# Optimization experiments

Hardware: AMD Instinct MI355X
Metric: run time of the kernel (lower is better)

Reference implementation:

```python
import jax, jax.numpy as jnp
import numpy as np
from jax import lax

B, T, L, OUT, SP, E, H = 128, 300, 28, 28, 7, 20, 256
W = T - L + 1          # 273 sliding windows
W_OUT = W - OUT        # 245 training windows
F_IN = L + 1 + E       # 49 rnn input features


def _lstm_dilated(x, d, Wih, Whh, b):
    # x: [T0, B, F]; dilation d realized by phase-stacking time into batch (zalando DRNN scheme)
    T0, Bn, F = x.shape
    pad = (-T0) % d
    if pad:
        x = jnp.concatenate([x, jnp.zeros((pad, Bn, F), x.dtype)], axis=0)
    Tn = x.shape[0] // d
    xd = x.reshape(Tn, d * Bn, F)  # element [k, j*Bn:(j+1)*Bn] == x[k*d+j]
    Hh = Whh.shape[1]

    def step(carry, xt):
        h, c = carry
        z = xt @ Wih.T + h @ Whh.T + b
        i, f, g, o = jnp.split(z, 4, axis=-1)  # torch LSTM gate order i,f,g,o
        c = jax.nn.sigmoid(f) * c + jax.nn.sigmoid(i) * jnp.tanh(g)
        h = jax.nn.sigmoid(o) * jnp.tanh(c)
        return (h, c), h

    h0 = jnp.zeros((d * Bn, Hh), x.dtype)
    _, hs = lax.scan(step, (h0, h0), xd)
    return hs.reshape(Tn * d, Bn, Hh)[:T0]


def _forward(train_dataset, val_dataset, alpha_raw, gamma_raw, init_seas,
             input_categories, my_param,
             Wih1, Whh1, b1, Wih2, Whh2, b2, Wih3, Whh3, b3, Wih4, Whh4, b4,
             linear_W, linear_b, score_W, score_b):
    x = train_dataset
    a = jax.nn.sigmoid(alpha_raw)   # [B]
    g = jax.nn.sigmoid(gamma_raw)   # [B]
    S0 = jnp.exp(init_seas)         # [B,7] = seasonalities[0..6]
    s7 = S0[:, 0]                   # seasonalities[7] = exp(init[:,0])
    level0 = x[:, 0] / S0[:, 0]
    buf0 = jnp.concatenate([S0[:, 1:], s7[:, None]], axis=1)  # S[1..7], shift register

    def es_step(carry, xt):
        level, buf = carry
        s = buf[:, 0]
        lvl = a * (xt / s) + (1.0 - a) * level
        s_new = g * (xt / lvl) + (1.0 - g) * s
        buf = jnp.concatenate([buf[:, 1:], s_new[:, None]], axis=1)
        return (lvl, buf), (lvl, s_new)

    _, (lvls, s_news) = lax.scan(es_step, (level0, buf0), x[:, 1:].T)
    levels = jnp.concatenate([level0[None], lvls], axis=0).T        # [B,T]
    S_full = jnp.concatenate([S0, s7[:, None], s_news.T], axis=1)   # [B,T+7]
    # extension: cat(S_full, S_full[:, T : T-7+28])  -> [B, T+28]
    S_ext = jnp.concatenate([S_full, S_full[:, T:T - SP + OUT]], axis=1)

    # input windows (vectorized over all W window positions)
    widx = jnp.arange(W)[:, None] + jnp.arange(L)[None, :]          # [W,L]
    lvl_w = levels[:, L - 1 + jnp.arange(W)]                        # [B,W]
    norm_in = x[:, widx] / S_ext[:, widx] / lvl_w[:, :, None]       # [B,W,L]
    cats = jnp.broadcast_to(input_categories[:, None, :], (B, W, E))
    cat_in = jnp.concatenate([norm_in, cats], axis=2)[jnp.arange(B) % 10]  # original j%10 row pick
    mp = jnp.broadcast_to(my_param.reshape(1, 1, 1), (B, W, 1))
    window_input = jnp.transpose(jnp.concatenate([cat_in, mp], axis=2), (1, 0, 2))  # [W,B,F_IN]

    # output windows
    oidx = (L + jnp.arange(W_OUT))[:, None] + jnp.arange(OUT)[None, :]  # [W_OUT,OUT]
    lvl_o = levels[:, L - 1 + jnp.arange(W_OUT)]                        # [B,W_OUT]
    window_output = jnp.transpose(x[:, oidx] / S_ext[:, oidx] / lvl_o[:, :, None], (1, 0, 2))

    # residual dilated LSTM stack: block1 dilations (1,2); block2 dilations (2,6) + residual
    h1 = _lstm_dilated(window_input, 1, Wih1, Whh1, b1)
    h1 = _lstm_dilated(h1, 2, Wih2, Whh2, b2)
    h2 = _lstm_dilated(h1, 2, Wih3, Whh3, b3)
    h2 = _lstm_dilated(h2, 6, Wih4, Whh4, b4) + h1
    h = jnp.tanh(h2 @ linear_W.T + linear_b)
    rnn_out = h @ score_W.T + score_b                                   # [W,B,OUT]

    # LSTM stack is causal, so running on window_input[:-OUT] equals slicing the full run
    prediction_values = rnn_out[:-OUT]
    actual_values = window_output
    holdout = rnn_out[-1] * S_ext[:, -OUT:] * levels[:, -1:]
    holdout_prediction = holdout * (holdout > 0).astype(holdout.dtype)
    hav = val_dataset
    hav_norm = hav / S_ext[:, -OUT:] / levels[:, -1:]
    return (prediction_values, actual_values, holdout_prediction, rnn_out, hav, hav_norm)


def setup_inputs() -> dict:
    key = jax.random.key(0)
    ks = jax.random.split(key, 24)
    s = float(1.0 / np.sqrt(H))
    u = lambda k, shape: jax.random.uniform(k, shape, jnp.float32, -s, s)
    inp = {
        "train_dataset": jax.random.uniform(ks[0], (B, T), jnp.float32) * 2.0 + 0.5,  # positive sales
        "val_dataset": jax.random.uniform(ks[1], (B, OUT), jnp.float32) * 2.0 + 0.5,
        "alpha_raw": jnp.full((B,), 0.5, jnp.float32),
        "gamma_raw": jnp.full((B,), 0.5, jnp.float32),
        "init_seas": jnp.full((B, SP), 0.5, jnp.float32),
        "input_categories": jnp.full((B, E), 0.001, jnp.float32) + 0.01 * jax.random.normal(ks[2], (B, E), jnp.float32),
        "my_param": jnp.full((1,), 0.001, jnp.float32),
        "Wih1": u(ks[3], (4 * H, F_IN)), "Whh1": u(ks[4], (4 * H, H)), "b1": u(ks[5], (4 * H,)),
        "Wih2": u(ks[6], (4 * H, H)), "Whh2": u(ks[7], (4 * H, H)), "b2": u(ks[8], (4 * H,)),
        "Wih3": u(ks[9], (4 * H, H)), "Whh3": u(ks[10], (4 * H, H)), "b3": u(ks[11], (4 * H,)),
        "Wih4": u(ks[12], (4 * H, H)), "Whh4": u(ks[13], (4 * H, H)), "b4": u(ks[14], (4 * H,)),
        "linear_W": u(ks[15], (H, H)), "linear_b": u(ks[16], (H,)),
        "score_W": u(ks[17], (OUT, H)), "score_b": u(ks[18], (OUT,)),
    }
    return inp


def reference(train_dataset, val_dataset, alpha_raw, gamma_raw, init_seas,
              input_categories, my_param,
              Wih1, Whh1, b1, Wih2, Whh2, b2, Wih3, Whh3, b3, Wih4, Whh4, b4,
              linear_W, linear_b, score_W, score_b):
    return _forward(train_dataset, val_dataset, alpha_raw, gamma_raw, init_seas,
                    input_categories, my_param,
                    Wih1, Whh1, b1, Wih2, Whh2, b2, Wih3, Whh3, b3, Wih4, Whh4, b4,
                    linear_W, linear_b, score_W, score_b)
```

## Files before the change

kernel.cpp:

```cpp
#include <hip/hip_runtime.h>

typedef unsigned int u32;

static __device__ __forceinline__ float sigf (float x){ return 1.0f/(1.0f+__expf(-x)); }
static __device__ __forceinline__ float tanh_(float x){ return 2.0f/(1.0f+__expf(-2.0f*x)) - 1.0f; }

#define NM 2730
#define N_O0 878080

static __device__ __forceinline__ int dot4(u32 a, u32 b, int acc){
#if __has_builtin(__builtin_amdgcn_sdot4)
  return __builtin_amdgcn_sdot4((int)a, (int)b, acc, false);
#else
  int s = acc;
  #pragma unroll
  for(int i=0;i<4;i++){
    int av = (int)((signed char)((a >> (8*i)) & 0xffu));
    int bv = (int)((signed char)((b >> (8*i)) & 0xffu));
    s += av*bv;
  }
  return s;
#endif
}

__global__ __launch_bounds__(256) void k_prep(
    const float* __restrict__ x,     float* __restrict__ xT,
    const float* __restrict__ wi0,   float* __restrict__ wT0,
    const float* __restrict__ wi1,   float* __restrict__ wT1,
    const float* __restrict__ wi2,   float* __restrict__ wT2,
    const float* __restrict__ wi3,   float* __restrict__ wT3,
    const float* __restrict__ lw,    float* __restrict__ lwT,
    const float* __restrict__ sw,    float* __restrict__ swT,
    const float* __restrict__ h0, const float* __restrict__ h1,
    const float* __restrict__ h2, const float* __restrict__ h3,
    float* __restrict__ zsc){
  int i = blockIdx.x*256 + threadIdx.x;
  if(i < 38400){
    int t = i >> 7, b = i & 127;
    xT[i] = x[b*300 + t];
    return;
  }
  i -= 38400;
  if(i < 50176){ int c=i/1024, r=i-c*1024; wT0[i] = wi0[r*49 + c];  return; }
  i -= 50176;
  if(i < 262144){ int c=i>>10, r=i&1023; wT1[i] = wi1[r*256 + c];   return; }
  i -= 262144;
  if(i < 262144){ int c=i>>10, r=i&1023; wT2[i] = wi2[r*256 + c];   return; }
  i -= 262144;
  if(i < 262144){ int c=i>>10, r=i&1023; wT3[i] = wi3[r*256 + c];   return; }
  i -= 262144;
  if(i < 65536){ int c=i>>8, r=i&255; lwT[i] = lw[r*256 + c];       return; }
  i -= 65536;
  if(i < 7168){ int c=i/28, r=i-c*28; swT[i] = sw[r*256 + c];       return; }
  i -= 7168;
  if(i < 4096){
    int l = i >> 10, r = i & 1023;
    const float* W = (l==0)?h0:(l==1)?h1:(l==2)?h2:h3;
    const float4* p = (const float4*)(W + (size_t)r*256);
    float m = 0.f;
    #pragma unroll 8
    for(int q=0;q<64;q++){
      float4 v = p[q];
      m = fmaxf(m, fmaxf(fmaxf(fabsf(v.x),fabsf(v.y)), fmaxf(fabsf(v.z),fabsf(v.w))));
    }
    zsc[i] = fmaxf(m, 1e-20f) * (1.0f/16129.0f);
  }
}

__global__ __launch_bounds__(256) void k_packes(
    const float* __restrict__ h0, const float* __restrict__ h1,
    const float* __restrict__ h2, const float* __restrict__ h3,
    const float* __restrict__ zsc, u32* __restrict__ W8,
    const float* __restrict__ xT, const float* __restrict__ alpha,
    const float* __restrict__ gamma, const float* __restrict__ iseas,
    float* __restrict__ ST, float* __restrict__ lvlT){
  __shared__ float xs[128*301];
  if(blockIdx.x < 1024){
    int i = blockIdx.x*256 + threadIdx.x;
    int l = i >> 16;
    int uidx = i & 65535;
    int dw = uidx & 3;
    int kg = (uidx >> 2) & 127;
    int q  = (uidx >> 9) & 3;
    int rr = (uidx >> 11) & 7;
    int js = uidx >> 14;
    int row = rr*128 + kg;
    int k0  = js*64 + q*16 + dw*4;
    const float* W = (l==0)?h0:(l==1)?h1:(l==2)?h2:h3;
    float inv = 1.0f / (zsc[l*1024 + row] * 127.0f);
    u32 out = 0;
    #pragma unroll
    for(int b=0;b<4;b++){
      float v = W[(size_t)row*256 + k0 + b];
      int q8 = max(-127, min(127, __float2int_rn(v * inv)));
      out |= ((u32)(q8 & 0xff)) << (8*b);
    }
    W8[i] = out;
    return;
  }
  for(int i=threadIdx.x; i<38400; i+=256){
    int t = i >> 7, b = i & 127;
    xs[b*301 + t] = xT[i];
  }
  __syncthreads();
  int b = threadIdx.x;
  if(b >= 128) return;
  float a = sigf(alpha[b]);
  float g = sigf(gamma[b]);
  float S0[7];
  #pragma unroll
  for(int i=0;i<7;i++){ S0[i] = __expf(iseas[b*7+i]); ST[i*128+b] = S0[i]; }
  ST[7*128+b] = S0[0];
  float q0=S0[1],q1=S0[2],q2=S0[3],q3=S0[4],q4=S0[5],q5=S0[6],q6=S0[0];
  float lvl = xs[b*301]/S0[0];
  lvlT[b] = lvl;
  for(int t=1;t<300;t++){
    float xt = xs[b*301 + t];
    float s  = q0;
    lvl = a*(xt/s) + (1.0f-a)*lvl;
    float sn = g*(xt/lvl) + (1.0f-g)*s;
    q0=q1;q1=q2;q2=q3;q3=q4;q4=q5;q5=q6;q6=sn;
    lvlT[t*128+b]   = lvl;
    ST[(t+7)*128+b] = sn;
  }
}

__global__ __launch_bounds__(256) void k_gemm1(
    const float* __restrict__ xT, const float* __restrict__ ST,
    const float* __restrict__ lvlT, const float* __restrict__ cats,
    const float* __restrict__ mp,
    const float* __restrict__ WT,
    const float* __restrict__ bias,
    float* __restrict__ Z){
  __shared__ float Xs[8][52];
  const int tid = threadIdx.x;
  const int m0 = blockIdx.x*8;
  for(int idx=tid; idx<8*49; idx+=256){
    int p = idx/49, f = idx - p*49;
    int m = m0+p;
    float v = 0.f;
    if(m < NM){
      int tt = m/10, jj = m - (m/10)*10;
      if(f < 28){
        int c = tt + f;
        v = xT[c*128 + jj] / ST[c*128 + jj] / lvlT[(tt+27)*128 + jj];
      } else if(f < 48){
        v = cats[jj*20 + (f-28)];
      } else {
        v = mp[0];
      }
    }
    Xs[p][f] = v;
  }
  __syncthreads();
  float acc0[8], acc1[8], acc2[8], acc3[8];
  {
    float b0 = bias[tid];
    float b1 = bias[tid+256];
    float b2 = bias[tid+512];
    float b3 = bias[tid+768];
    #pragma unroll
    for(int p=0;p<8;p++){ acc0[p]=b0; acc1[p]=b1; acc2[p]=b2; acc3[p]=b3; }
  }
  #pragma unroll 7
  for(int f=0; f<49; f++){
    float w0 = WT[f*1024 + tid      ];
    float w1 = WT[f*1024 + tid+256  ];
    float w2 = WT[f*1024 + tid+512  ];
    float w3 = WT[f*1024 + tid+768  ];
    #pragma unroll
    for(int p=0;p<8;p++){
      float xv = Xs[p][f];
      acc0[p] += w0*xv; acc1[p] += w1*xv; acc2[p] += w2*xv; acc3[p] += w3*xv;
    }
  }
  for(int p=0;p<8;p++){
    int m = m0+p;
    if(m < NM){
      float* zb = Z + m*1024 + tid;
      zb[0]=acc0[p]; zb[256]=acc1[p]; zb[512]=acc2[p]; zb[768]=acc3[p];
    }
  }
}

__global__ __launch_bounds__(256) void k_gemm(const float* __restrict__ X,
                                              const float* __restrict__ WT,
                                              const float* __restrict__ bias,
                                              float* __restrict__ Z){
  __shared__ float Xs[8][256];
  const int tid = threadIdx.x;
  const int m0 = blockIdx.x*8;
  for(int p=0;p<8;p++){
    int m = m0+p;
    Xs[p][tid] = (m < NM) ? X[m*256+tid] : 0.0f;
  }
  __syncthreads();
  float acc0[8], acc1[8], acc2[8], acc3[8];
  {
    float b0 = bias[tid];
    float b1 = bias[tid+256];
    float b2 = bias[tid+512];
    float b3 = bias[tid+768];
    #pragma unroll
    for(int p=0;p<8;p++){ acc0[p]=b0; acc1[p]=b1; acc2[p]=b2; acc3[p]=b3; }
  }
  #pragma unroll 4
  for(int f=0; f<256; f++){
    float w0 = WT[f*1024 + tid      ];
    float w1 = WT[f*1024 + tid+256  ];
    float w2 = WT[f*1024 + tid+512  ];
    float w3 = WT[f*1024 + tid+768  ];
    #pragma unroll
    for(int p=0;p<8;p++){
      float xv = Xs[p][f];
      acc0[p] += w0*xv; acc1[p] += w1*xv; acc2[p] += w2*xv; acc3[p] += w3*xv;
    }
  }
  for(int p=0;p<8;p++){
    int m = m0+p;
    if(m < NM){
      float* zb = Z + m*1024 + tid;
      zb[0]=acc0[p]; zb[256]=acc1[p]; zb[512]=acc2[p]; zb[768]=acc3[p];
    }
  }
}

__global__ __launch_bounds__(512) void k_scan8(
    const float* __restrict__ Z,
    const u32* __restrict__ W8,
    const float* __restrict__ zsc,
    float* __restrict__ Y,
    const float* __restrict__ RES,
    int d){
  __shared__ __align__(16) u32 h8[64];
  __shared__ int   zp[4][1024];
  __shared__ float sc[1024];
  const int tid = threadIdx.x;
  const int chain = blockIdx.x;
  const int j = chain % 10;
  const int r = chain / 10;
  const int ns = (273 - r + d - 1)/d;
  const int kg = tid & 127;
  const int js = tid >> 7;
  const uint4* Wb = (const uint4*)W8 + (size_t)js*4096 + kg;
  const uint4* hq = (const uint4*)h8 + js*4;

  for(int i=tid;i<1024;i+=512) sc[i] = zsc[i];
  if(tid < 64) h8[tid] = 0u;
  float cst = 0.0f;
  __syncthreads();

  int t = r;
  for(int s=0; s<ns; s++, t+=d){
    const size_t row = (size_t)(t*10 + j);
    float zv0=0.f, zv1=0.f, zv2=0.f, zv3=0.f, rv=0.f;
    if(tid < 256){
      const float* zb = Z + row*1024;
      zv0 = zb[tid]; zv1 = zb[tid+256]; zv2 = zb[tid+512]; zv3 = zb[tid+768];
      if(RES) rv = RES[row*256 + tid];
    }
    int a0=0,a1=0,a2=0,a3=0,a4=0,a5=0,a6=0,a7=0;
    #pragma unroll
    for(int q=0;q<4;q++){
      uint4 h4 = hq[q];
      #pragma unroll
      for(int rr=0;rr<8;rr++){
        uint4 w = Wb[rr*512 + q*128];
        int* ap = (rr==0)?&a0:(rr==1)?&a1:(rr==2)?&a2:(rr==3)?&a3:
                  (rr==4)?&a4:(rr==5)?&a5:(rr==6)?&a6:&a7;
        int acc = *ap;
        acc = dot4(w.x, h4.x, acc);
        acc = dot4(w.y, h4.y, acc);
        acc = dot4(w.z, h4.z, acc);
        acc = dot4(w.w, h4.w, acc);
        *ap = acc;
      }
    }
    zp[js][       kg] = a0;
    zp[js][128  + kg] = a1;
    zp[js][256  + kg] = a2;
    zp[js][384  + kg] = a3;
    zp[js][512  + kg] = a4;
    zp[js][640  + kg] = a5;
    zp[js][768  + kg] = a6;
    zp[js][896  + kg] = a7;
    __syncthreads();
    if(tid < 256){
      const int u = tid;
      int si = zp[0][u]     + zp[1][u]     + zp[2][u]     + zp[3][u];
      int sf = zp[0][u+256] + zp[1][u+256] + zp[2][u+256] + zp[3][u+256];
      int sg = zp[0][u+512] + zp[1][u+512] + zp[2][u+512] + zp[3][u+512];
      int so = zp[0][u+768] + zp[1][u+768] + zp[2][u+768] + zp[3][u+768];
      float zi = zv0 + sc[u]     * (float)si;
      float zf = zv1 + sc[u+256] * (float)sf;
      float zg = zv2 + sc[u+512] * (float)sg;
      float zo = zv3 + sc[u+768] * (float)so;
      float c  = sigf(zf)*cst + sigf(zi)*tanh_(zg);
      float h  = sigf(zo)*tanh_(c);
      cst = c;
      int hqi = __float2int_rn(h * 127.0f);
      hqi = max(-127, min(127, hqi));
      ((signed char*)h8)[u] = (signed char)hqi;
      Y[row*256 + u] = h + rv;
    }
    asm volatile("s_waitcnt lgkmcnt(0)\n\ts_barrier" ::: "memory");
  }
}

__global__ __launch_bounds__(256) void k_head(const float* __restrict__ Y4,
    const float* __restrict__ LWT,
    const float* __restrict__ lb,
    const float* __restrict__ SWT,
    const float* __restrict__ sb,
    float* __restrict__ rnnS){
  __shared__ float v [8][256];
  __shared__ float h2[8][256];
  const int tid = threadIdx.x;
  const int m0 = blockIdx.x*8;
  for(int p=0;p<8;p++){
    int m = m0+p;
    v[p][tid] = (m<NM) ? Y4[m*256+tid] : 0.0f;
  }
  __syncthreads();
  float acc[8];
  float bz = lb[tid];
  #pragma unroll
  for(int p=0;p<8;p++) acc[p]=bz;
  #pragma unroll 4
  for(int f=0; f<256; f++){
    float w = LWT[f*256+tid];
    #pragma unroll
    for(int p=0;p<8;p++) acc[p] += w * v[p][f];
  }
  #pragma unroll
  for(int p=0;p<8;p++) h2[p][tid] = tanh_(acc[p]);
  __syncthreads();
  if(tid < 224){
    int o = tid % 28, p = tid / 28;
    int m = m0 + p;
    if(m < NM){
      float a = sb[o];
      for(int f=0; f<256; f++) a += SWT[f*28+o] * h2[p][f];
      rnnS[m*28 + o] = a;
    }
  }
}

__global__ __launch_bounds__(256) void k_outs(
    const float* __restrict__ rnnS, const float* __restrict__ ST,
    const float* __restrict__ lvlT, const float* __restrict__ xT,
    const float* __restrict__ val,  float* __restrict__ out,
    int nblk){
  const int tid = threadIdx.x;
  const int bid = blockIdx.x;
  if(bid < 245){
    __shared__ float av[28*132];
    const int t = bid;
    for(int i=tid; i<28*128; i+=256){
      int o = i >> 7, b = i & 127;
      int c = 28 + t + o;
      av[o*132 + b] = xT[c*128+b] / ST[c*128+b] / lvlT[(27+t)*128+b];
    }
    __syncthreads();
    for(int i=tid; i<3584; i+=256){
      int b = i/28, o = i - b*28;
      out[878080 + t*3584 + i] = av[o*132 + b];
    }
    return;
  }
  const int stride = (nblk - 245)*256;
  for(int i0 = (bid-245)*256 + tid; i0 < 978432 + 3584 + 3584; i0 += stride){
    int i = i0;
    if(i < 978432){
      int t = i/3584; int rr = i - t*3584;
      int b = rr/28;  int o = rr - b*28;
      int j = b % 10;
      float a = rnnS[(t*10 + j)*28 + o];
      out[1759744 + i] = a;
      if(t < 245) out[i] = a;
    } else { i -= 978432;
      if(i < 3584){
        int b = i/28, o = i - (i/28)*28;
        int j = b % 10;
        float a = rnnS[(2720 + j)*28 + o];
        int col = (o < 21) ? (286+o) : (279+o);
        float hv = a * ST[col*128 + b] * lvlT[299*128 + b];
        out[1756160 + i] = (hv > 0.0f) ? hv : 0.0f;
      } else { i -= 3584;
        int b = i/28, o = i - (i/28)*28;
        int col = (o < 21) ? (286+o) : (279+o);
        float Sm = ST[col*128 + b];
        float lv = lvlT[299*128 + b];
        out[2738176 + i] = val[i];
        out[2741760 + i] = val[i] / Sm / lv;
      }
    }
  }
}

extern "C" void kernel_launch(void* const* d_in, const int* in_sizes, int n_in,
                              void* d_out, int out_size, void* d_ws, size_t ws_size,
                              hipStream_t stream){
  (void)in_sizes; (void)n_in; (void)out_size; (void)ws_size;
  const float* x     = (const float*)d_in[0];
  const float* val   = (const float*)d_in[1];
  const float* alpha = (const float*)d_in[2];
  const float* gamma = (const float*)d_in[3];
  const float* iseas = (const float*)d_in[4];
  const float* cats  = (const float*)d_in[5];
  const float* mp    = (const float*)d_in[6];
  const float* Wih[4]  = {(const float*)d_in[7],  (const float*)d_in[10], (const float*)d_in[13], (const float*)d_in[16]};
  const float* Whh[4]  = {(const float*)d_in[8],  (const float*)d_in[11], (const float*)d_in[14], (const float*)d_in[17]};
  const float* bias[4] = {(const float*)d_in[9],  (const float*)d_in[12], (const float*)d_in[15], (const float*)d_in[18]};
  const float* linW  = (const float*)d_in[19];
  const float* linb  = (const float*)d_in[20];
  const float* scW   = (const float*)d_in[21];
  const float* scb   = (const float*)d_in[22];

  float* Fw   = (float*)d_ws;
  float* ST   = Fw;
  float* lvlT = ST   + 39296;
  float* xT   = lvlT + 38400;
  float* xz   = xT   + 38400;
  float* yA   = xz   + 2795520;
  float* yB   = yA   + 698880;
  float* wihT[4];
  wihT[0] = yB + 698880;
  wihT[1] = wihT[0] + 50176;
  wihT[2] = wihT[1] + 262144;
  wihT[3] = wihT[2] + 262144;
  float* linWT = wihT[3] + 262144;
  float* scT   = linWT + 65536;
  float* zsc   = scT   + 7168;
  u32*   W8all = (u32*)(zsc + 4096);
  float* rnnS  = (float*)(W8all + 262144);

  k_prep<<<3718, 256, 0, stream>>>(x, xT,
      Wih[0], wihT[0], Wih[1], wihT[1], Wih[2], wihT[2], Wih[3], wihT[3],
      linW, linWT, scW, scT,
      Whh[0], Whh[1], Whh[2], Whh[3], zsc);

  k_packes<<<1025, 256, 0, stream>>>(Whh[0], Whh[1], Whh[2], Whh[3], zsc, W8all,
                                     xT, alpha, gamma, iseas, ST, lvlT);

  const int    dlt[4]    = {1, 2, 2, 6};
  const int    chains[4] = {10, 20, 20, 60};
  const float* Xin[4]    = {nullptr, yA, yB, yA};
  float*       Yout[4]   = {yA, yB, yA, yA};
  for(int l=0;l<4;l++){
    if(l == 0)
      k_gemm1<<<(NM+7)/8, 256, 0, stream>>>(xT, ST, lvlT, cats, mp,
                                            wihT[0], bias[0], xz);
    else
      k_gemm<<<(NM+7)/8, 256, 0, stream>>>(Xin[l], wihT[l], bias[l], xz);
    k_scan8<<<chains[l], 512, 0, stream>>>(xz, W8all + l*65536, zsc + l*1024,
                                           Yout[l],
                                           (l==3) ? yB : (const float*)nullptr, dlt[l]);
  }

  k_head<<<(NM+7)/8, 256, 0, stream>>>(yA, linWT, linb, scT, scb, rnnS);
  const int nblk = 245 + 1024;
  k_outs<<<nblk, 256, 0, stream>>>(rnnS, ST, lvlT, xT, val, (float*)d_out, nblk);
}
```

Measured before the change: 958.6 us.

## Fuse prep kernels, merge per-layer GEMM and scan with flag sync

Measured after the change: 1.026 ms. +7.0%, slower.

```diff
diff --git a/kernel.cpp b/kernel.cpp
--- a/kernel.cpp
+++ b/kernel.cpp
@@ -23,220 +23,195 @@
 #endif
 }
 
-__global__ __launch_bounds__(256) void k_prep(
-    const float* __restrict__ x,     float* __restrict__ xT,
-    const float* __restrict__ wi0,   float* __restrict__ wT0,
-    const float* __restrict__ wi1,   float* __restrict__ wT1,
-    const float* __restrict__ wi2,   float* __restrict__ wT2,
-    const float* __restrict__ wi3,   float* __restrict__ wT3,
-    const float* __restrict__ lw,    float* __restrict__ lwT,
-    const float* __restrict__ sw,    float* __restrict__ swT,
+__global__ __launch_bounds__(256) void k_prepall(
+    const float* __restrict__ x,
+    const float* __restrict__ alpha, const float* __restrict__ gamma,
+    const float* __restrict__ iseas,
+    const float* __restrict__ wi0, const float* __restrict__ wi1,
+    const float* __restrict__ wi2, const float* __restrict__ wi3,
+    const float* __restrict__ lw,  const float* __restrict__ sw,
     const float* __restrict__ h0, const float* __restrict__ h1,
     const float* __restrict__ h2, const float* __restrict__ h3,
-    float* __restrict__ zsc){
-  int i = blockIdx.x*256 + threadIdx.x;
-  if(i < 38400){
-    int t = i >> 7, b = i & 127;
-    xT[i] = x[b*300 + t];
+    float* __restrict__ xT,  float* __restrict__ wT0, float* __restrict__ wT1,
+    float* __restrict__ wT2, float* __restrict__ wT3,
+    float* __restrict__ lwT, float* __restrict__ swT,
+    float* __restrict__ zsc, u32* __restrict__ W8,
+    float* __restrict__ ST, float* __restrict__ lvlT,
+    u32* __restrict__ flags){
+  __shared__ float xs[128*61];
+  const int tid = threadIdx.x;
+  const int bid = blockIdx.x;
+  if(bid == 0){
+    int b = tid;
+    float a=0.f, g=0.f, lvl=0.f;
+    float q0=0,q1=0,q2=0,q3=0,q4=0,q5=0,q6=0;
+    if(tid < 128){
+      a = sigf(alpha[b]);
+      g = sigf(gamma[b]);
+      float S0[7];
+      #pragma unroll
+      for(int i=0;i<7;i++){ S0[i] = __expf(iseas[b*7+i]); ST[i*128+b] = S0[i]; }
+      ST[7*128+b] = S0[0];
+      q0=S0[1];q1=S0[2];q2=S0[3];q3=S0[4];q4=S0[5];q5=S0[6];q6=S0[0];
+      lvl = 0.f;
+      (void)lvl;
+    }
+    for(int c=0;c<5;c++){
+      __syncthreads();
+      for(int i=tid; i<128*60; i+=256){
+        int bb = i/60, tt = i - bb*60;
+        xs[bb*61 + tt] = x[bb*300 + c*60 + tt];
+      }
+      __syncthreads();
+      if(tid < 128){
+        int tt0 = 0;
+        if(c == 0){
+          lvl = xs[b*61] / q6;
+          lvlT[b] = lvl;
+          tt0 = 1;
+        }
+        for(int tt=tt0; tt<60; tt++){
+          int t = c*60 + tt;
+          float xt = xs[b*61 + tt];
+          float s  = q0;
+          lvl = a*(xt/s) + (1.0f-a)*lvl;
+          float sn = g*(xt/lvl) + (1.0f-g)*s;
+          q0=q1;q1=q2;q2=q3;q3=q4;q4=q5;q5=q6;q6=sn;
+          lvlT[t*128+b]   = lvl;
+          ST[(t+7)*128+b] = sn;
+        }
+      }
+    }
     return;
   }
+  if(bid <= 1024){
+    if(bid == 1 && tid < 4) flags[tid] = 0u;
+    int gid  = (bid-1)*4 + (tid >> 6);
+    int lane = tid & 63;
+    int l    = gid >> 10;
+    int row  = gid & 1023;
+    const float* W = (l==0)?h0:(l==1)?h1:(l==2)?h2:h3;
+    float4 v = ((const float4*)(W + (size_t)row*256))[lane];
+    float m = fmaxf(fmaxf(fabsf(v.x),fabsf(v.y)), fmaxf(fabsf(v.z),fabsf(v.w)));
+    #pragma unroll
+    for(int d=1; d<64; d<<=1) m = fmaxf(m, __shfl_xor(m, d));
+    float zv = fmaxf(m, 1e-20f) * (1.0f/16129.0f);
+    if(lane == 0) zsc[gid] = zv;
+    float inv = 1.0f / (zv * 127.0f);
+    u32 out = 0;
+    {
+      float vv[4] = {v.x, v.y, v.z, v.w};
+      #pragma unroll
+      for(int bq=0;bq<4;bq++){
+        int q8 = max(-127, min(127, __float2int_rn(vv[bq] * inv)));
+        out |= ((u32)(q8 & 0xff)) << (8*bq);
+      }
+    }
+    int js = lane >> 4, q = (lane >> 2) & 3, dw = lane & 3;
+    W8[(size_t)l*65536 + js*16384 + (row>>7)*2048 + q*512 + (row&127)*4 + dw] = out;
+    return;
+  }
+  int i = (bid-1025)*256 + tid;
+  if(i < 38400){ int t=i>>7, b=i&127; xT[i] = x[b*300+t]; return; }
   i -= 38400;
-  if(i < 50176){ int c=i/1024, r=i-c*1024; wT0[i] = wi0[r*49 + c];  return; }
+  if(i < 50176){ int c=i/1024, r=i-c*1024; wT0[i] = wi0[r*49+c]; return; }
   i -= 50176;
-  if(i < 262144){ int c=i>>10, r=i&1023; wT1[i] = wi1[r*256 + c];   return; }
+  if(i < 262144){ int c=i>>10, r=i&1023; wT1[i] = wi1[r*256+c]; return; }
   i -= 262144;
-  if(i < 262144){ int c=i>>10, r=i&1023; wT2[i] = wi2[r*256 + c];   return; }
+  if(i < 262144){ int c=i>>10, r=i&1023; wT2[i] = wi2[r*256+c]; return; }
   i -= 262144;
-  if(i < 262144){ int c=i>>10, r=i&1023; wT3[i] = wi3[r*256 + c];   return; }
+  if(i < 262144){ int c=i>>10, r=i&1023; wT3[i] = wi3[r*256+c]; return; }
   i -= 262144;
-  if(i < 65536){ int c=i>>8, r=i&255; lwT[i] = lw[r*256 + c];       return; }
+  if(i < 65536){ int c=i>>8, r=i&255; lwT[i] = lw[r*256+c]; return; }
   i -= 65536;
-  if(i < 7168){ int c=i/28, r=i-c*28; swT[i] = sw[r*256 + c];       return; }
-  i -= 7168;
-  if(i < 4096){
-    int l = i >> 10, r = i & 1023;
-    const float* W = (l==0)?h0:(l==1)?h1:(l==2)?h2:h3;
-    const float4* p = (const float4*)(W + (size_t)r*256);
-    float m = 0.f;
-    #pragma unroll 8
-    for(int q=0;q<64;q++){
-      float4 v = p[q];
-      m = fmaxf(m, fmaxf(fmaxf(fabsf(v.x),fabsf(v.y)), fmaxf(fabsf(v.z),fabsf(v.w))));
-    }
-    zsc[i] = fmaxf(m, 1e-20f) * (1.0f/16129.0f);
-  }
-}
-
-__global__ __launch_bounds__(256) void k_packes(
-    const float* __restrict__ h0, const float* __restrict__ h1,
-    const float* __restrict__ h2, const float* __restrict__ h3,
-    const float* __restrict__ zsc, u32* __restrict__ W8,
-    const float* __restrict__ xT, const float* __restrict__ alpha,
-    const float* __restrict__ gamma, const float* __restrict__ iseas,
-    float* __restrict__ ST, float* __restrict__ lvlT){
-  __shared__ float xs[128*301];
-  if(blockIdx.x < 1024){
-    int i = blockIdx.x*256 + threadIdx.x;
-    int l = i >> 16;
-    int uidx = i & 65535;
-    int dw = uidx & 3;
-    int kg = (uidx >> 2) & 127;
-    int q  = (uidx >> 9) & 3;
-    int rr = (uidx >> 11) & 7;
-    int js = uidx >> 14;
-    int row = rr*128 + kg;
-    int k0  = js*64 + q*16 + dw*4;
-    const float* W = (l==0)?h0:(l==1)?h1:(l==2)?h2:h3;
-    float inv = 1.0f / (zsc[l*1024 + row] * 127.0f);
-    u32 out = 0;
-    #pragma unroll
-    for(int b=0;b<4;b++){
-      float v = W[(size_t)row*256 + k0 + b];
-      int q8 = max(-127, min(127, __float2int_rn(v * inv)));
-      out |= ((u32)(q8 & 0xff)) << (8*b);
-    }
-    W8[i] = out;
-    return;
-  }
-  for(int i=threadIdx.x; i<38400; i+=256){
-    int t = i >> 7, b = i & 127;
-    xs[b*301 + t] = xT[i];
-  }
-  __syncthreads();
-  int b = threadIdx.x;
-  if(b >= 128) return;
-  float a = sigf(alpha[b]);
-  float g = sigf(gamma[b]);
-  float S0[7];
-  #pragma unroll
-  for(int i=0;i<7;i++){ S0[i] = __expf(iseas[b*7+i]); ST[i*128+b] = S0[i]; }
-  ST[7*128+b] = S0[0];
-  float q0=S0[1],q1=S0[2],q2=S0[3],q3=S0[4],q4=S0[5],q5=S0[6],q6=S0[0];
-  float lvl = xs[b*301]/S0[0];
-  lvlT[b] = lvl;
-  for(int t=1;t<300;t++){
-    float xt = xs[b*301 + t];
-    float s  = q0;
-    lvl = a*(xt/s) + (1.0f-a)*lvl;
-    float sn = g*(xt/lvl) + (1.0f-g)*s;
-    q0=q1;q1=q2;q2=q3;q3=q4;q4=q5;q5=q6;q6=sn;
-    lvlT[t*128+b]   = lvl;
-    ST[(t+7)*128+b] = sn;
-  }
-}
-
-__global__ __launch_bounds__(256) void k_gemm1(
+  if(i < 7168){ int c=i/28, r=i-c*28; swT[i] = sw[r*256+c]; }
+}
+
+__global__ __launch_bounds__(512) void k_gs(
+    const float* __restrict__ X,
     const float* __restrict__ xT, const float* __restrict__ ST,
     const float* __restrict__ lvlT, const float* __restrict__ cats,
     const float* __restrict__ mp,
-    const float* __restrict__ WT,
-    const float* __restrict__ bias,
-    float* __restrict__ Z){
-  __shared__ float Xs[8][52];
+    const float* __restrict__ WT, const float* __restrict__ bias,
+    float* __restrict__ Z,
+    const u32* __restrict__ W8, const float* __restrict__ zsc,
+    float* __restrict__ Y, const float* __restrict__ RES,
+    u32* __restrict__ flag,
+    int first, int chains, int d){
+  __shared__ __align__(16) char arena[21504];
   const int tid = threadIdx.x;
-  const int m0 = blockIdx.x*8;
-  for(int idx=tid; idx<8*49; idx+=256){
-    int p = idx/49, f = idx - p*49;
-    int m = m0+p;
-    float v = 0.f;
-    if(m < NM){
-      int tt = m/10, jj = m - (m/10)*10;
-      if(f < 28){
-        int c = tt + f;
-        v = xT[c*128 + jj] / ST[c*128 + jj] / lvlT[(tt+27)*128 + jj];
-      } else if(f < 48){
-        v = cats[jj*20 + (f-28)];
-      } else {
-        v = mp[0];
-      }
-    }
-    Xs[p][f] = v;
+  const int bid = blockIdx.x;
+  if(bid < 171){
+    float* Xs = (float*)arena;
+    const int m0 = bid*16;
+    const int XSTR = first ? 52 : 256;
+    if(first){
+      for(int idx=tid; idx<16*49; idx+=512){
+        int p = idx/49, f = idx - p*49;
+        int m = m0+p;
+        float v = 0.f;
+        if(m < NM){
+          int tt = m/10, jj = m - (m/10)*10;
+          if(f < 28){
+            int c = tt + f;
+            v = xT[c*128+jj] / ST[c*128+jj] / lvlT[(tt+27)*128+jj];
+          } else if(f < 48){
+            v = cats[jj*20 + (f-28)];
+          } else {
+            v = mp[0];
+          }
+        }
+        Xs[p*XSTR + f] = v;
+      }
+    } else {
+      for(int idx=tid; idx<16*256; idx+=512){
+        int p = idx >> 8, c = idx & 255;
+        int m = m0+p;
+        Xs[p*XSTR + c] = (m < NM) ? X[(size_t)m*256 + c] : 0.f;
+      }
+    }
+    __syncthreads();
+    float a0[16], a1[16];
+    {
+      float b0 = bias[tid], b1 = bias[tid+512];
+      #pragma unroll
+      for(int p=0;p<16;p++){ a0[p]=b0; a1[p]=b1; }
+    }
+    const int K = first ? 49 : 256;
+    #pragma unroll 4
+    for(int f=0; f<K; f++){
+      float w0 = WT[f*1024 + tid];
+      float w1 = WT[f*1024 + tid + 512];
+      #pragma unroll
+      for(int p=0;p<16;p++){
+        float xv = Xs[p*XSTR + f];
+        a0[p] += w0*xv; a1[p] += w1*xv;
+      }
+    }
+    for(int p=0;p<16;p++){
+      int m = m0+p;
+      if(m < NM){
+        float* zb = Z + (size_t)m*1024;
+        zb[tid] = a0[p]; zb[tid+512] = a1[p];
+      }
+    }
+    __syncthreads();
+    __threadfence();
+    if(tid == 0)
+      __hip_atomic_fetch_add(flag, 1u, __ATOMIC_RELEASE, __HIP_MEMORY_SCOPE_AGENT);
+    return;
+  }
+  const int chain = bid - 171;
+  if(chain >= chains) return;
+  u32*   h8 = (u32*)arena;
+  int*   zp = (int*)(arena + 256);
+  float* sc = (float*)(arena + 256 + 16384);
+  if(tid == 0){
+    while(__hip_atomic_load(flag, __ATOMIC_RELAXED, __HIP_MEMORY_SCOPE_AGENT) < 171u)
+      __builtin_amdgcn_s_sleep(8);
   }
   __syncthreads();
-  float acc0[8], acc1[8], acc2[8], acc3[8];
-  {
-    float b0 = bias[tid];
-    float b1 = bias[tid+256];
-    float b2 = bias[tid+512];
-    float b3 = bias[tid+768];
-    #pragma unroll
-    for(int p=0;p<8;p++){ acc0[p]=b0; acc1[p]=b1; acc2[p]=b2; acc3[p]=b3; }
-  }
-  #pragma unroll 7
-  for(int f=0; f<49; f++){
-    float w0 = WT[f*1024 + tid      ];
-    float w1 = WT[f*1024 + tid+256  ];
-    float w2 = WT[f*1024 + tid+512  ];
-    float w3 = WT[f*1024 + tid+768  ];
-    #pragma unroll
-    for(int p=0;p<8;p++){
-      float xv = Xs[p][f];
-      acc0[p] += w0*xv; acc1[p] += w1*xv; acc2[p] += w2*xv; acc3[p] += w3*xv;
-    }
-  }
-  for(int p=0;p<8;p++){
-    int m = m0+p;
-    if(m < NM){
-      float* zb = Z + m*1024 + tid;
-      zb[0]=acc0[p]; zb[256]=acc1[p]; zb[512]=acc2[p]; zb[768]=acc3[p];
-    }
-  }
-}
-
-__global__ __launch_bounds__(256) void k_gemm(const float* __restrict__ X,
-                                              const float* __restrict__ WT,
-                                              const float* __restrict__ bias,
-                                              float* __restrict__ Z){
-  __shared__ float Xs[8][256];
-  const int tid = threadIdx.x;
-  const int m0 = blockIdx.x*8;
-  for(int p=0;p<8;p++){
-    int m = m0+p;
-    Xs[p][tid] = (m < NM) ? X[m*256+tid] : 0.0f;
-  }
-  __syncthreads();
-  float acc0[8], acc1[8], acc2[8], acc3[8];
-  {
-    float b0 = bias[tid];
-    float b1 = bias[tid+256];
-    float b2 = bias[tid+512];
-    float b3 = bias[tid+768];
-    #pragma unroll
-    for(int p=0;p<8;p++){ acc0[p]=b0; acc1[p]=b1; acc2[p]=b2; acc3[p]=b3; }
-  }
-  #pragma unroll 4
-  for(int f=0; f<256; f++){
-    float w0 = WT[f*1024 + tid      ];
-    float w1 = WT[f*1024 + tid+256  ];
-    float w2 = WT[f*1024 + tid+512  ];
-    float w3 = WT[f*1024 + tid+768  ];
-    #pragma unroll
-    for(int p=0;p<8;p++){
-      float xv = Xs[p][f];
-      acc0[p] += w0*xv; acc1[p] += w1*xv; acc2[p] += w2*xv; acc3[p] += w3*xv;
-    }
-  }
-  for(int p=0;p<8;p++){
-    int m = m0+p;
-    if(m < NM){
-      float* zb = Z + m*1024 + tid;
-      zb[0]=acc0[p]; zb[256]=acc1[p]; zb[512]=acc2[p]; zb[768]=acc3[p];
-    }
-  }
-}
-
-__global__ __launch_bounds__(512) void k_scan8(
-    const float* __restrict__ Z,
-    const u32* __restrict__ W8,
-    const float* __restrict__ zsc,
-    float* __restrict__ Y,
-    const float* __restrict__ RES,
-    int d){
-  __shared__ __align__(16) u32 h8[64];
-  __shared__ int   zp[4][1024];
-  __shared__ float sc[1024];
-  const int tid = threadIdx.x;
-  const int chain = blockIdx.x;
+  __builtin_amdgcn_fence(__ATOMIC_ACQUIRE, "agent");
   const int j = chain % 10;
   const int r = chain / 10;
   const int ns = (273 - r + d - 1)/d;
@@ -276,21 +251,21 @@
         *ap = acc;
       }
     }
-    zp[js][       kg] = a0;
-    zp[js][128  + kg] = a1;
-    zp[js][256  + kg] = a2;
-    zp[js][384  + kg] = a3;
-    zp[js][512  + kg] = a4;
-    zp[js][640  + kg] = a5;
-    zp[js][768  + kg] = a6;
-    zp[js][896  + kg] = a7;
+    zp[js*1024 +       kg] = a0;
+    zp[js*1024 + 128 + kg] = a1;
+    zp[js*1024 + 256 + kg] = a2;
+    zp[js*1024 + 384 + kg] = a3;
+    zp[js*1024 + 512 + kg] = a4;
+    zp[js*1024 + 640 + kg] = a5;
+    zp[js*1024 + 768 + kg] = a6;
+    zp[js*1024 + 896 + kg] = a7;
     __syncthreads();
     if(tid < 256){
       const int u = tid;
-      int si = zp[0][u]     + zp[1][u]     + zp[2][u]     + zp[3][u];
-      int sf = zp[0][u+256] + zp[1][u+256] + zp[2][u+256] + zp[3][u+256];
-      int sg = zp[0][u+512] + zp[1][u+512] + zp[2][u+512] + zp[3][u+512];
-      int so = zp[0][u+768] + zp[1][u+768] + zp[2][u+768] + zp[3][u+768];
+      int si = zp[u]     + zp[1024+u]     + zp[2048+u]     + zp[3072+u];
+      int sf = zp[u+256] + zp[1024+u+256] + zp[2048+u+256] + zp[3072+u+256];
+      int sg = zp[u+512] + zp[1024+u+512] + zp[2048+u+512] + zp[3072+u+512];
+      int so = zp[u+768] + zp[1024+u+768] + zp[2048+u+768] + zp[3072+u+768];
       float zi = zv0 + sc[u]     * (float)si;
       float zf = zv1 + sc[u+256] * (float)sf;
       float zg = zv2 + sc[u+512] * (float)sg;
@@ -307,55 +282,51 @@
   }
 }
 
-__global__ __launch_bounds__(256) void k_head(const float* __restrict__ Y4,
-    const float* __restrict__ LWT,
-    const float* __restrict__ lb,
-    const float* __restrict__ SWT,
-    const float* __restrict__ sb,
-    float* __restrict__ rnnS){
-  __shared__ float v [8][256];
-  __shared__ float h2[8][256];
-  const int tid = threadIdx.x;
-  const int m0 = blockIdx.x*8;
-  for(int p=0;p<8;p++){
-    int m = m0+p;
-    v[p][tid] = (m<NM) ? Y4[m*256+tid] : 0.0f;
-  }
-  __syncthreads();
-  float acc[8];
-  float bz = lb[tid];
-  #pragma unroll
-  for(int p=0;p<8;p++) acc[p]=bz;
-  #pragma unroll 4
-  for(int f=0; f<256; f++){
-    float w = LWT[f*256+tid];
-    #pragma unroll
-    for(int p=0;p<8;p++) acc[p] += w * v[p][f];
-  }
-  #pragma unroll
-  for(int p=0;p<8;p++) h2[p][tid] = tanh_(acc[p]);
-  __syncthreads();
-  if(tid < 224){
-    int o = tid % 28, p = tid / 28;
-    int m = m0 + p;
-    if(m < NM){
-      float a = sb[o];
-      for(int f=0; f<256; f++) a += SWT[f*28+o] * h2[p][f];
-      rnnS[m*28 + o] = a;
-    }
-  }
-}
-
-__global__ __launch_bounds__(256) void k_outs(
-    const float* __restrict__ rnnS, const float* __restrict__ ST,
-    const float* __restrict__ lvlT, const float* __restrict__ xT,
-    const float* __restrict__ val,  float* __restrict__ out,
-    int nblk){
+__global__ __launch_bounds__(256) void k_headav(const float* __restrict__ Y4,
+    const float* __restrict__ LWT, const float* __restrict__ lb,
+    const float* __restrict__ SWT, const float* __restrict__ sb,
+    const float* __restrict__ ST, const float* __restrict__ lvlT,
+    const float* __restrict__ xT, const float* __restrict__ val,
+    float* __restrict__ rnnS, float* __restrict__ out){
+  __shared__ float arena[4224];
   const int tid = threadIdx.x;
   const int bid = blockIdx.x;
-  if(bid < 245){
-    __shared__ float av[28*132];
-    const int t = bid;
+  if(bid < 342){
+    float* v  = arena;
+    float* h2 = arena + 2048;
+    const int m0 = bid*8;
+    for(int p=0;p<8;p++){
+      int m = m0+p;
+      v[p*256+tid] = (m<NM) ? Y4[m*256+tid] : 0.0f;
+    }
+    __syncthreads();
+    float acc[8];
+    float bz = lb[tid];
+    #pragma unroll
+    for(int p=0;p<8;p++) acc[p]=bz;
+    #pragma unroll 4
+    for(int f=0; f<256; f++){
+      float w = LWT[f*256+tid];
+      #pragma unroll
+      for(int p=0;p<8;p++) acc[p] += w * v[p*256+f];
+    }
+    #pragma unroll
+    for(int p=0;p<8;p++) h2[p*256+tid] = tanh_(acc[p]);
+    __syncthreads();
+    if(tid < 224){
+      int o = tid % 28, p = tid / 28;
+      int m = m0 + p;
+      if(m < NM){
+        float a = sb[o];
+        for(int f=0; f<256; f++) a += SWT[f*28+o] * h2[p*256+f];
+        rnnS[m*28 + o] = a;
+      }
+    }
+    return;
+  }
+  if(bid < 587){
+    float* av = arena;
+    const int t = bid - 342;
     for(int i=tid; i<28*128; i+=256){
       int o = i >> 7, b = i & 127;
       int c = 28 + t + o;
@@ -368,8 +339,20 @@
     }
     return;
   }
-  const int stride = (nblk - 245)*256;
-  for(int i0 = (bid-245)*256 + tid; i0 < 978432 + 3584 + 3584; i0 += stride){
+  for(int i=tid; i<3584; i+=256){
+    int b = i/28, o = i%28;
+    int col = (o < 21) ? (286+o) : (279+o);
+    float Sm = ST[col*128 + b];
+    float lv = lvlT[299*128 + b];
+    out[2738176 + i] = val[i];
+    out[2741760 + i] = val[i] / Sm / lv;
+  }
+}
+
+__global__ __launch_bounds__(256) void k_bcast(
+    const float* __restrict__ rnnS, const float* __restrict__ ST,
+    const float* __restrict__ lvlT, float* __restrict__ out){
+  for(int i0 = blockIdx.x*256 + threadIdx.x; i0 < 978432 + 3584; i0 += 1024*256){
     int i = i0;
     if(i < 978432){
       int t = i/3584; int rr = i - t*3584;
@@ -379,21 +362,12 @@
       out[1759744 + i] = a;
       if(t < 245) out[i] = a;
     } else { i -= 978432;
-      if(i < 3584){
-        int b = i/28, o = i - (i/28)*28;
-        int j = b % 10;
-        float a = rnnS[(2720 + j)*28 + o];
-        int col = (o < 21) ? (286+o) : (279+o);
-        float hv = a * ST[col*128 + b] * lvlT[299*128 + b];
-        out[1756160 + i] = (hv > 0.0f) ? hv : 0.0f;
-      } else { i -= 3584;
-        int b = i/28, o = i - (i/28)*28;
-        int col = (o < 21) ? (286+o) : (279+o);
-        float Sm = ST[col*128 + b];
-        float lv = lvlT[299*128 + b];
-        out[2738176 + i] = val[i];
-        out[2741760 + i] = val[i] / Sm / lv;
-      }
+      int b = i/28, o = i - (i/28)*28;
+      int j = b % 10;
+      float a = rnnS[(2720 + j)*28 + o];
+      int col = (o < 21) ? (286+o) : (279+o);
+      float hv = a * ST[col*128 + b] * lvlT[299*128 + b];
+      out[1756160 + i] = (hv > 0.0f) ? hv : 0.0f;
     }
   }
 }
@@ -434,31 +408,28 @@
   float* zsc   = scT   + 7168;
   u32*   W8all = (u32*)(zsc + 4096);
   float* rnnS  = (float*)(W8all + 262144);
-
-  k_prep<<<3718, 256, 0, stream>>>(x, xT,
-      Wih[0], wihT[0], Wih[1], wihT[1], Wih[2], wihT[2], Wih[3], wihT[3],
-      linW, linWT, scW, scT,
-      Whh[0], Whh[1], Whh[2], Whh[3], zsc);
-
-  k_packes<<<1025, 256, 0, stream>>>(Whh[0], Whh[1], Whh[2], Whh[3], zsc, W8all,
-                                     xT, alpha, gamma, iseas, ST, lvlT);
+  u32*   flags = (u32*)(rnnS + 76440);
+
+  k_prepall<<<4727, 256, 0, stream>>>(x, alpha, gamma, iseas,
+      Wih[0], Wih[1], Wih[2], Wih[3], linW, scW,
+      Whh[0], Whh[1], Whh[2], Whh[3],
+      xT, wihT[0], wihT[1], wihT[2], wihT[3], linWT, scT,
+      zsc, W8all, ST, lvlT, flags);
 
   const int    dlt[4]    = {1, 2, 2, 6};
   const int    chains[4] = {10, 20, 20, 60};
   const float* Xin[4]    = {nullptr, yA, yB, yA};
   float*       Yout[4]   = {yA, yB, yA, yA};
   for(int l=0;l<4;l++){
-    if(l == 0)
-      k_gemm1<<<(NM+7)/8, 256, 0, stream>>>(xT, ST, lvlT, cats, mp,
-                                            wihT[0], bias[0], xz);
-    else
-      k_gemm<<<(NM+7)/8, 256, 0, stream>>>(Xin[l], wihT[l], bias[l], xz);
-    k_scan8<<<chains[l], 512, 0, stream>>>(xz, W8all + l*65536, zsc + l*1024,
-                                           Yout[l],
-                                           (l==3) ? yB : (const float*)nullptr, dlt[l]);
-  }
-
-  k_head<<<(NM+7)/8, 256, 0, stream>>>(yA, linWT, linb, scT, scb, rnnS);
-  const int nblk = 245 + 1024;
-  k_outs<<<nblk, 256, 0, stream>>>(rnnS, ST, lvlT, xT, val, (float*)d_out, nblk);
-}
+    k_gs<<<171 + chains[l], 512, 0, stream>>>(
+        Xin[l], xT, ST, lvlT, cats, mp,
+        wihT[l], bias[l], xz,
+        W8all + l*65536, zsc + l*1024,
+        Yout[l], (l==3) ? yB : (const float*)nullptr,
+        flags + l, (l==0) ? 1 : 0, chains[l], dlt[l]);
+  }
+
+  k_headav<<<588, 256, 0, stream>>>(yA, linWT, linb, scT, scb,
+                                    ST, lvlT, xT, val, rnnS, (float*)d_out);
+  k_bcast<<<1024, 256, 0, stream>>>(rnnS, ST, lvlT, (float*)d_out);
+}
```
